# Kernel optimization log

Hardware: AMD Instinct MI355X
Metric: run time of the kernel (lower is better)

Reference implementation:

```python
import jax, jax.numpy as jnp
import numpy as np

# -------- static graph construction (Traffic4cast-style pixel grid) --------
H, W = 495, 436
N = H * W                    # 215820 nodes
D_NODE, D_EDGE, UNITS = 128, 32, 128
UQ = UNITS // 4              # per-quadrant width (combination='concat')
SCALE = 1.0 / 4.0            # 1/(max_neighbors+1)

def _first_occ_unique(v):
    """tf.unique semantics: unique values in first-occurrence order + idx map."""
    u, first, inv = np.unique(v, return_index=True, return_inverse=True)
    order = np.argsort(first)
    rank = np.empty(len(u), dtype=np.int64)
    rank[order] = np.arange(len(u))
    return u[order], rank[inv]

def _build_graph():
    r, c = np.meshgrid(np.arange(H), np.arange(W), indexing='ij')
    node_loc = np.stack([r.ravel(), c.ravel()], -1).astype(np.int64)
    def grid_edges(r0, r1, c0, c1, dr, dc):
        rr, cc = np.meshgrid(np.arange(r0, r1), np.arange(c0, c1), indexing='ij')
        src = (rr * W + cc).ravel()
        dst = ((rr + dr) * W + (cc + dc)).ravel()
        return np.stack([src, dst], -1).astype(np.int64)
    eis = [grid_edges(1, H, 0, W, -1, 0),   # north
           grid_edges(0, H, 0, W - 1, 0, 1),# east
           grid_edges(0, H - 1, 0, W, 1, 0),# south
           grid_edges(0, H, 1, W, 0, -1)]   # west
    return node_loc, eis

NODE_LOC, EIS = _build_graph()

# --- graph_pooling_2x2 bucketing (col_idx=0): pos_id = (r//2)*half_cols + c//2 ---
_half_cols = NODE_LOC[:, 0].max() + 1
_pos_id = (NODE_LOC // 2 * np.array([_half_cols, 1])).sum(-1)
_, NEW_NODE_IDS = _first_occ_unique(_pos_id)
N_POOLED = int(NEW_NODE_IDS.max()) + 1

# --- remove_duplicate_edges precompute per direction (static, int-only) ---
EDGE_SEG, K_UNIQ, KEEP_IDX, NEW_EIDX = [], [], [], []
for _ei in EIS:
    _pe = NEW_NODE_IDS[_ei]
    _lin = _pe[:, 0] * N + _pe[:, 1]
    _u, _seg = _first_occ_unique(_lin)
    _ne = np.stack([_u // N, _u % N], -1)
    _keep = np.where(_ne[:, 0] != _ne[:, 1])[0]
    EDGE_SEG.append(_seg)
    K_UNIQ.append(len(_u))
    KEEP_IDX.append(_keep)
    NEW_EIDX.append(_ne[_keep])


def setup_inputs() -> dict:
    key = jax.random.key(0)
    ks = jax.random.split(key, 9)
    inp = {
        'x': jax.random.normal(ks[0], (N, D_NODE), dtype=jnp.float32),
        'node_loc': jnp.asarray(NODE_LOC),
        'edge_index_n': jnp.asarray(EIS[0]),
        'edge_index_e': jnp.asarray(EIS[1]),
        'edge_index_s': jnp.asarray(EIS[2]),
        'edge_index_w': jnp.asarray(EIS[3]),
        'edges_n': jax.random.uniform(ks[1], (EIS[0].shape[0], D_EDGE), dtype=jnp.float32),
        'edges_e': jax.random.uniform(ks[2], (EIS[1].shape[0], D_EDGE), dtype=jnp.float32),
        'edges_s': jax.random.uniform(ks[3], (EIS[2].shape[0], D_EDGE), dtype=jnp.float32),
        'edges_w': jax.random.uniform(ks[4], (EIS[3].shape[0], D_EDGE), dtype=jnp.float32),
        'W_emb': jax.random.normal(ks[5], (4, D_NODE, UQ), dtype=jnp.float32) * 0.05,
        'W_edge': jax.random.normal(ks[6], (4, D_EDGE + 2 * UQ, UQ), dtype=jnp.float32) * 0.05,
        'W_node': jax.random.normal(ks[7], (D_NODE + UNITS, UNITS), dtype=jnp.float32) * 0.05,
    }
    return inp


def reference(x, node_loc, edge_index_n, edge_index_e, edge_index_s, edge_index_w,
              edges_n, edges_e, edges_s, edges_w, W_emb, W_edge, W_node):
    n = x.shape[0]
    eis = (edge_index_n, edge_index_e, edge_index_s, edge_index_w)
    efs = (edges_n, edges_e, edges_s, edges_w)
    aggs, quad_edges = [], []
    # GeoQuadrantGCN.call_concat (use_global=False, use_bias=False, relu)
    for q in range(4):
        ei = eis[q]
        xq = jax.nn.relu(x @ W_emb[q])                              # [N, UQ]
        edge_in = jnp.concatenate([efs[q], xq[ei[:, 0]], xq[ei[:, 1]]], axis=-1)
        edge = jax.nn.relu(edge_in @ W_edge[q])                     # [E, UQ]
        aggs.append(jax.ops.segment_sum(edge, ei[:, 1], num_segments=n) * SCALE)
        quad_edges.append(edge)
    x2 = jax.nn.relu(jnp.concatenate([x] + aggs, axis=-1) @ W_node) # [N, UNITS]
    # graph_pooling_2x2
    x_pooled = jax.ops.segment_max(x2, jnp.asarray(NEW_NODE_IDS), num_segments=N_POOLED)
    new_pos = jax.ops.segment_min(node_loc // 2, jnp.asarray(NEW_NODE_IDS), num_segments=N_POOLED)
    new_efeats = [
        jax.ops.segment_max(quad_edges[q], jnp.asarray(EDGE_SEG[q]), num_segments=K_UNIQ[q])[KEEP_IDX[q]]
        for q in range(4)
    ]
    new_eidx = [jnp.asarray(NEW_EIDX[q]) for q in range(4)]
    return (x_pooled, new_pos, *new_eidx, *new_efeats)
```

## Files before the change

### kernel.cpp

```cpp
#include <hip/hip_runtime.h>

#define NN 215820
#define NPOOL 54064
#define KN 53846
#define KE 53816

static constexpr size_t OFF_POS = (size_t)NPOOL * 128;
static constexpr size_t OFF_EIN = OFF_POS + (size_t)NPOOL * 2;
static constexpr size_t OFF_EIE = OFF_EIN + (size_t)KN * 2;
static constexpr size_t OFF_EIS = OFF_EIE + (size_t)KE * 2;
static constexpr size_t OFF_EIW = OFF_EIS + (size_t)KN * 2;
static constexpr size_t OFF_EFN = OFF_EIW + (size_t)KE * 2;
static constexpr size_t OFF_EFE = OFF_EFN + (size_t)KN * 32;
static constexpr size_t OFF_EFS = OFF_EFE + (size_t)KE * 32;
static constexpr size_t OFF_EFW = OFF_EFS + (size_t)KN * 32;

typedef __attribute__((ext_vector_type(8))) short  short8v;
typedef __attribute__((ext_vector_type(4))) float  floatx4;

__device__ __align__(16) unsigned short g_wn_h[128 * 256];
__device__ __align__(16) unsigned short g_wn_l[128 * 256];

__device__ __forceinline__ void bf16split(float x, unsigned short& h,
                                          unsigned short& l) {
  const unsigned int u = __float_as_uint(x);
  h = (unsigned short)(u >> 16);
  const float hf = __uint_as_float(u & 0xffff0000u);
  l = (unsigned short)(__float_as_uint(x - hf) >> 16);
}

__device__ __forceinline__ void gemm_chunk(const float* __restrict__ xs,
                                           const float* __restrict__ ws,
                                           const float* const xr[8],
                                           int tx4, float acc[8][8]) {
#pragma unroll 1
  for (int kb = 0; kb < 32; kb += 4) {
    float4 xv[8];
#pragma unroll
    for (int i = 0; i < 8; ++i) xv[i] = *(const float4*)(xr[i] + kb);
    float4 wl[4], wh[4];
#pragma unroll
    for (int kk = 0; kk < 4; ++kk) {
      wl[kk] = *(const float4*)(ws + (kb + kk) * 132 + tx4);
      wh[kk] = *(const float4*)(ws + (kb + kk) * 132 + tx4 + 64);
    }
#pragma unroll
    for (int i = 0; i < 8; ++i) {
      const float* xe = (const float*)&xv[i];
#pragma unroll
      for (int kk = 0; kk < 4; ++kk) {
        acc[i][0] = fmaf(xe[kk], wl[kk].x, acc[i][0]);
        acc[i][1] = fmaf(xe[kk], wl[kk].y, acc[i][1]);
        acc[i][2] = fmaf(xe[kk], wl[kk].z, acc[i][2]);
        acc[i][3] = fmaf(xe[kk], wl[kk].w, acc[i][3]);
        acc[i][4] = fmaf(xe[kk], wh[kk].x, acc[i][4]);
        acc[i][5] = fmaf(xe[kk], wh[kk].y, acc[i][5]);
        acc[i][6] = fmaf(xe[kk], wh[kk].z, acc[i][6]);
        acc[i][7] = fmaf(xe[kk], wh[kk].w, acc[i][7]);
      }
    }
  }
}

__global__ __launch_bounds__(256) void k_xq(const float* __restrict__ x,
                                            const float* __restrict__ W_emb,
                                            float* __restrict__ xq) {
  __shared__ float xs[128 * 36];
  __shared__ float ws[32 * 132];
  const int t  = threadIdx.x;
  const int tx = t & 15, ty = t >> 4;
  const int n0 = blockIdx.x * 128;
  const int srow = t >> 1, soff = (t & 1) * 16;
  int snode = n0 + srow; if (snode >= NN) snode = NN - 1;
  const float* sxa = x + (size_t)snode * 128 + soff;
  float* sxd = xs + srow * 36 + soff;

  int rowidx[8];
#pragma unroll
  for (int i = 0; i < 4; ++i) { rowidx[i] = 4 * ty + i; rowidx[4 + i] = 64 + 4 * ty + i; }
  const float* xr[8];
#pragma unroll
  for (int i = 0; i < 8; ++i) xr[i] = xs + rowidx[i] * 36;
  const int tx4 = tx * 4;

  float acc[8][8];
#pragma unroll
  for (int i = 0; i < 8; ++i)
#pragma unroll
    for (int j = 0; j < 8; ++j) acc[i][j] = 0.f;

  for (int kc = 0; kc < 4; ++kc) {
    __syncthreads();
#pragma unroll
    for (int i = 0; i < 4; ++i)
      *(float4*)(sxd + 4 * i) = *(const float4*)(sxa + kc * 32 + 4 * i);
#pragma unroll
    for (int i = 0; i < 4; ++i) {
      const int f = t * 16 + 4 * i, kk = f >> 7, c = f & 127;
      *(float4*)(ws + kk * 132 + c) =
          *(const float4*)(W_emb + (size_t)(c >> 5) * 4096 +
                           (size_t)(kc * 32 + kk) * 32 + (c & 31));
    }
    __syncthreads();
    gemm_chunk(xs, ws, xr, tx4, acc);
  }
  const int qlo = tx >> 3, ulo = tx4 & 31;
#pragma unroll
  for (int i = 0; i < 8; ++i) {
    const int n = n0 + rowidx[i];
    if (n < NN) {
      float4 v, u;
      v.x = fmaxf(acc[i][0], 0.f); v.y = fmaxf(acc[i][1], 0.f);
      v.z = fmaxf(acc[i][2], 0.f); v.w = fmaxf(acc[i][3], 0.f);
      u.x = fmaxf(acc[i][4], 0.f); u.y = fmaxf(acc[i][5], 0.f);
      u.z = fmaxf(acc[i][6], 0.f); u.w = fmaxf(acc[i][7], 0.f);
      *(float4*)(xq + ((size_t)qlo * NN + n) * 32 + ulo) = v;
      *(float4*)(xq + ((size_t)(qlo + 2) * NN + n) * 32 + ulo) = u;
    }
  }
}

__global__ __launch_bounds__(256, 4) void k_node(const float* __restrict__ x,
                                                 const float* __restrict__ agg,
                                                 float* __restrict__ out) {
  __shared__ short As_h[128 * 32], As_l[128 * 32];
  __shared__ short Bs_h[128 * 32], Bs_l[128 * 32];
  const int t   = threadIdx.x;
  const int pr  = blockIdx.y;
  const int pc0 = blockIdx.x * 32;

  const int srow = t >> 1, q0 = t & 1;
  int ra = (srow < 64) ? 2 * pr : 2 * pr + 1; if (ra > 494) ra = 494;
  int ca = 2 * pc0 + (srow & 63);          if (ca > 435) ca = 435;
  const size_t snode = (size_t)ra * 436 + ca;

  const int w = t >> 6, lane = t & 63;
  const int lr = lane & 15, lg = lane >> 4;

  floatx4 acc[2][8];
#pragma unroll
  for (int mi = 0; mi < 2; ++mi)
#pragma unroll
    for (int ni = 0; ni < 8; ++ni) acc[mi][ni] = (floatx4){0.f, 0.f, 0.f, 0.f};

  for (int ks = 0; ks < 8; ++ks) {
    __syncthreads();
    const float* src = (ks < 4) ? (x + snode * 128 + ks * 32)
                                : (agg + snode * 128 + (ks - 4) * 32);
#pragma unroll
    for (int cc = 0; cc < 2; ++cc) {
      const int q = q0 + 2 * cc;
      const floatx4 v0 = *(const floatx4*)(src + q * 8);
      const floatx4 v1 = *(const floatx4*)(src + q * 8 + 4);
      short8v hv, lv;
#pragma unroll
      for (int j = 0; j < 4; ++j) {
        unsigned short h, l;
        bf16split(v0[j], h, l); hv[j] = (short)h; lv[j] = (short)l;
        bf16split(v1[j], h, l); hv[4 + j] = (short)h; lv[4 + j] = (short)l;
      }
      const int off = srow * 64 + ((q * 16) ^ ((srow & 3) << 4));
      *(short8v*)((char*)As_h + off) = hv;
      *(short8v*)((char*)As_l + off) = lv;
      const size_t wb = (size_t)srow * 256 + ks * 32 + q * 8;
      *(short8v*)((char*)Bs_h + off) = *(const short8v*)(g_wn_h + wb);
      *(short8v*)((char*)Bs_l + off) = *(const short8v*)(g_wn_l + wb);
    }
    __syncthreads();
    short8v ah[2], al[2];
#pragma unroll
    for (int mi = 0; mi < 2; ++mi) {
      const int row = (mi ? 64 : 0) + 16 * w + lr;
      const int off = row * 64 + ((lg * 16) ^ ((row & 3) << 4));
      ah[mi] = *(const short8v*)((const char*)As_h + off);
      al[mi] = *(const short8v*)((const char*)As_l + off);
    }
#pragma unroll
    for (int ni = 0; ni < 8; ++ni) {
      const int col = 16 * ni + lr;
      const int off = col * 64 + ((lg * 16) ^ ((col & 3) << 4));
      const short8v bh = *(const short8v*)((const char*)Bs_h + off);
      const short8v bl = *(const short8v*)((const char*)Bs_l + off);
#pragma unroll
      for (int mi = 0; mi < 2; ++mi) {
        acc[mi][ni] = __builtin_amdgcn_mfma_f32_16x16x32_bf16(ah[mi], bh, acc[mi][ni], 0, 0, 0);
        acc[mi][ni] = __builtin_amdgcn_mfma_f32_16x16x32_bf16(ah[mi], bl, acc[mi][ni], 0, 0, 0);
        acc[mi][ni] = __builtin_amdgcn_mfma_f32_16x16x32_bf16(al[mi], bh, acc[mi][ni], 0, 0, 0);
      }
    }
  }
#pragma unroll
  for (int ni = 0; ni < 8; ++ni) {
#pragma unroll
    for (int k = 0; k < 2; ++k) {
      float v = fmaxf(fmaxf(acc[0][ni][2 * k], acc[0][ni][2 * k + 1]),
                      fmaxf(acc[1][ni][2 * k], acc[1][ni][2 * k + 1]));
      v = fmaxf(v, 0.f);
      const int pc = pc0 + 8 * w + 2 * lg + k;
      if (pc < 218) out[((size_t)pr * 218 + pc) * 128 + 16 * ni + lr] = v;
    }
  }
}

__global__ __launch_bounds__(256) void k_edge(
    const float* __restrict__ ef_n, const float* __restrict__ ef_e,
    const float* __restrict__ ef_s, const float* __restrict__ ef_w,
    const float* __restrict__ xq, const float* __restrict__ W_edge,
    float* __restrict__ agg, float* __restrict__ out) {
  const int q = blockIdx.y;
  const float* ef; float* efb; int P;
  if (q == 0)      { ef = ef_n; P = 107692; efb = out + OFF_EFN; }
  else if (q == 1) { ef = ef_e; P = 107880; efb = out + OFF_EFE; }
  else if (q == 2) { ef = ef_s; P = 107692; efb = out + OFF_EFS; }
  else             { ef = ef_w; P = 107880; efb = out + OFF_EFW; }
  const int j = threadIdx.x & 31, slot = threadIdx.x >> 5;
  const float* Wq = W_edge + q * 3072;
  float wcol[96];
#pragma unroll
  for (int k = 0; k < 96; ++k) wcol[k] = Wq[k * 32 + j];
  const float* xqq = xq + (size_t)q * NN * 32;
  __shared__ float ein[8][192];
  float* row = ein[slot];

  for (int p = blockIdx.x * 8 + slot; p < P; p += gridDim.x * 8) {
    int e1, src1, dst1, e2, src2, dst2, kidx; bool kept, has2;
    if (q == 0) {
      const int rp = p / 218, pc = p - rp * 218;
      const int r = rp + 1, c = 2 * pc;
      e1 = (r - 1) * 436 + c; e2 = e1 + 1;
      src1 = r * 436 + c; dst1 = src1 - 436;
      src2 = src1 + 1; dst2 = dst1 + 1; has2 = true;
      kept = (r & 1) == 0; kidx = ((r >> 1) - 1) * 218 + pc;
    } else if (q == 2) {
      const int r = p / 218, pc = p - r * 218;
      const int c = 2 * pc;
      e1 = r * 436 + c; e2 = e1 + 1;
      src1 = e1; dst1 = src1 + 436;
      src2 = src1 + 1; dst2 = dst1 + 1; has2 = true;
      kept = (r & 1) == 1; kidx = (r >> 1) * 218 + pc;
    } else if (q == 1) {
      const int pr = p / 435, c = p - pr * 435;
      e1 = 2 * pr * 435 + c; e2 = e1 + 435;
      src1 = 2 * pr * 436 + c; dst1 = src1 + 1;
      src2 = src1 + 436; dst2 = dst1 + 436;
      has2 = pr < 247;
      kept = (c & 1) == 1; kidx = pr * 217 + (c >> 1);
    } else {
      const int pr = p / 435, cm = p - pr * 435;
      const int c = cm + 1;
      e1 = 2 * pr * 435 + cm; e2 = e1 + 435;
      src1 = 2 * pr * 436 + c; dst1 = src1 - 1;
      src2 = src1 + 436; dst2 = dst1 + 436;
      has2 = pr < 247;
      kept = (c & 1) == 0; kidx = pr * 217 + (c >> 1) - 1;
    }
    const int e2c = has2 ? e2 : e1;
    const int s2c = has2 ? src2 : src1;
    const int d2c = has2 ? dst2 : dst1;
    row[j]       = ef[(size_t)e1 * 32 + j];
    row[32 + j]  = xqq[(size_t)src1 * 32 + j];
    row[64 + j]  = xqq[(size_t)dst1 * 32 + j];
    row[96 + j]  = ef[(size_t)e2c * 32 + j];
    row[128 + j] = xqq[(size_t)s2c * 32 + j];
    row[160 + j] = xqq[(size_t)d2c * 32 + j];
    float a1 = 0.f, a2 = 0.f;
#pragma unroll
    for (int kq = 0; kq < 24; ++kq) {
      const float4 b1 = *(const float4*)&row[4 * kq];
      const float4 b2 = *(const float4*)&row[96 + 4 * kq];
      a1 = fmaf(b1.x, wcol[4 * kq + 0], a1); a1 = fmaf(b1.y, wcol[4 * kq + 1], a1);
      a1 = fmaf(b1.z, wcol[4 * kq + 2], a1); a1 = fmaf(b1.w, wcol[4 * kq + 3], a1);
      a2 = fmaf(b2.x, wcol[4 * kq + 0], a2); a2 = fmaf(b2.y, wcol[4 * kq + 1], a2);
      a2 = fmaf(b2.z, wcol[4 * kq + 2], a2); a2 = fmaf(b2.w, wcol[4 * kq + 3], a2);
    }
    const float f1 = fmaxf(a1, 0.f), f2 = fmaxf(a2, 0.f);
    agg[(size_t)dst1 * 128 + q * 32 + j] = f1 * 0.25f;
    if (has2) agg[(size_t)dst2 * 128 + q * 32 + j] = f2 * 0.25f;
    if (kept) efb[(size_t)kidx * 32 + j] = has2 ? fmaxf(f1, f2) : f1;
  }
}

__global__ __launch_bounds__(256) void k_misc(float* __restrict__ out,
                                              float* __restrict__ agg,
                                              const float* __restrict__ W_node) {
  int u = blockIdx.x * 256 + threadIdx.x;
  if (u < 436 * 32) {
    agg[((size_t)494 * 436 + (u >> 5)) * 128 + (u & 31)] = 0.f; return;
  }
  u -= 436 * 32;
  if (u < 495 * 32) {
    agg[(size_t)(u >> 5) * 436 * 128 + 32 + (u & 31)] = 0.f; return;
  }
  u -= 495 * 32;
  if (u < 436 * 32) {
    agg[(size_t)(u >> 5) * 128 + 64 + (u & 31)] = 0.f; return;
  }
  u -= 436 * 32;
  if (u < 495 * 32) {
    agg[((size_t)(u >> 5) * 436 + 435) * 128 + 96 + (u & 31)] = 0.f; return;
  }
  u -= 495 * 32;
  if (u < NPOOL * 2) {
    const int p  = u >> 1;
    const int pr = p / 218, pc = p - pr * 218;
    out[OFF_POS + u] = (float)((u & 1) ? pc : pr); return;
  }
  u -= NPOOL * 2;
  if (u < KN * 2) {
    const int e  = u >> 1;
    const int kr = e / 218 + 1, pc = e - (kr - 1) * 218;
    const int s  = kr * 218 + pc;
    out[OFF_EIN + u] = (float)((u & 1) ? (s - 218) : s); return;
  }
  u -= KN * 2;
  if (u < KE * 2) {
    const int e  = u >> 1;
    const int pr = e / 217, jj = e - pr * 217;
    const int s  = pr * 218 + jj;
    out[OFF_EIE + u] = (float)((u & 1) ? (s + 1) : s); return;
  }
  u -= KE * 2;
  if (u < KN * 2) {
    const int e  = u >> 1;
    const int k  = e / 218, pc = e - k * 218;
    const int s  = k * 218 + pc;
    out[OFF_EIS + u] = (float)((u & 1) ? (s + 218) : s); return;
  }
  u -= KN * 2;
  if (u < KE * 2) {
    const int e  = u >> 1;
    const int pr = e / 217, jj = e - pr * 217;
    const int s  = pr * 218 + jj + 1;
    out[OFF_EIW + u] = (float)((u & 1) ? (s - 1) : s); return;
  }
  u -= KE * 2;
  if (u < 256 * 128) {
    const int k = u >> 7, c = u & 127;
    unsigned short h, l;
    bf16split(W_node[u], h, l);
    g_wn_h[(size_t)c * 256 + k] = h;
    g_wn_l[(size_t)c * 256 + k] = l;
  }
}

extern "C" void kernel_launch(void* const* d_in, const int* in_sizes, int n_in,
                              void* d_out, int out_size, void* d_ws, size_t ws_size,
                              hipStream_t stream) {
  const float* x      = (const float*)d_in[0];
  const float* ef_n   = (const float*)d_in[6];
  const float* ef_e   = (const float*)d_in[7];
  const float* ef_s   = (const float*)d_in[8];
  const float* ef_w   = (const float*)d_in[9];
  const float* W_emb  = (const float*)d_in[10];
  const float* W_edge = (const float*)d_in[11];
  const float* W_node = (const float*)d_in[12];
  float* out = (float*)d_out;

  float* xq  = (float*)d_ws;
  float* agg = xq + (size_t)NN * 128;

  const int misc_total = (436 + 495 + 436 + 495) * 32 + NPOOL * 2 +
                         2 * (KN * 2 + KE * 2) + 256 * 128;
  k_misc<<<dim3((misc_total + 255) / 256), 256, 0, stream>>>(out, agg, W_node);
  k_xq  <<<dim3((NN + 127) / 128), 256, 0, stream>>>(x, W_emb, xq);
  k_edge<<<dim3(512, 4), 256, 0, stream>>>(ef_n, ef_e, ef_s, ef_w,
                                           xq, W_edge, agg, out);
  k_node<<<dim3(7, 248), 256, 0, stream>>>(x, agg, out);
}
```

Before: 509.7 us.

## Compute node embedding GEMM with split-bf16 MFMA instead of FP32 FMAs

The x @ W_emb kernel is rewritten to use bf16 MFMA instructions with a hi/lo split (three MFMAs per tile) in place of the scalar FP32 FMA tiling. W_emb is pre-split into transposed bf16 hi/lo arrays inside the misc kernel, and x is split on the fly into swizzled shared memory. This moves the embedding GEMM onto the matrix cores while keeping near-FP32 accuracy. In exchange the output stores become scalar rather than float4, and the extra split work adds ALU cost.

```diff
diff --git a/kernel.cpp b/kernel.cpp
--- a/kernel.cpp
+++ b/kernel.cpp
@@ -20,6 +20,8 @@
 
 __device__ __align__(16) unsigned short g_wn_h[128 * 256];
 __device__ __align__(16) unsigned short g_wn_l[128 * 256];
+__device__ __align__(16) unsigned short g_we_h[128 * 128];
+__device__ __align__(16) unsigned short g_we_l[128 * 128];
 
 __device__ __forceinline__ void bf16split(float x, unsigned short& h,
                                           unsigned short& l) {
@@ -29,93 +31,81 @@
   l = (unsigned short)(__float_as_uint(x - hf) >> 16);
 }
 
-__device__ __forceinline__ void gemm_chunk(const float* __restrict__ xs,
-                                           const float* __restrict__ ws,
-                                           const float* const xr[8],
-                                           int tx4, float acc[8][8]) {
-#pragma unroll 1
-  for (int kb = 0; kb < 32; kb += 4) {
-    float4 xv[8];
-#pragma unroll
-    for (int i = 0; i < 8; ++i) xv[i] = *(const float4*)(xr[i] + kb);
-    float4 wl[4], wh[4];
-#pragma unroll
-    for (int kk = 0; kk < 4; ++kk) {
-      wl[kk] = *(const float4*)(ws + (kb + kk) * 132 + tx4);
-      wh[kk] = *(const float4*)(ws + (kb + kk) * 132 + tx4 + 64);
-    }
-#pragma unroll
-    for (int i = 0; i < 8; ++i) {
-      const float* xe = (const float*)&xv[i];
-#pragma unroll
-      for (int kk = 0; kk < 4; ++kk) {
-        acc[i][0] = fmaf(xe[kk], wl[kk].x, acc[i][0]);
-        acc[i][1] = fmaf(xe[kk], wl[kk].y, acc[i][1]);
-        acc[i][2] = fmaf(xe[kk], wl[kk].z, acc[i][2]);
-        acc[i][3] = fmaf(xe[kk], wl[kk].w, acc[i][3]);
-        acc[i][4] = fmaf(xe[kk], wh[kk].x, acc[i][4]);
-        acc[i][5] = fmaf(xe[kk], wh[kk].y, acc[i][5]);
-        acc[i][6] = fmaf(xe[kk], wh[kk].z, acc[i][6]);
-        acc[i][7] = fmaf(xe[kk], wh[kk].w, acc[i][7]);
-      }
-    }
-  }
-}
-
-__global__ __launch_bounds__(256) void k_xq(const float* __restrict__ x,
-                                            const float* __restrict__ W_emb,
-                                            float* __restrict__ xq) {
-  __shared__ float xs[128 * 36];
-  __shared__ float ws[32 * 132];
+__global__ __launch_bounds__(256, 4) void k_xq(const float* __restrict__ x,
+                                               float* __restrict__ xq) {
+  __shared__ __align__(16) short As_h[128 * 32], As_l[128 * 32];
+  __shared__ __align__(16) short Bs_h[128 * 32], Bs_l[128 * 32];
   const int t  = threadIdx.x;
-  const int tx = t & 15, ty = t >> 4;
   const int n0 = blockIdx.x * 128;
-  const int srow = t >> 1, soff = (t & 1) * 16;
-  int snode = n0 + srow; if (snode >= NN) snode = NN - 1;
-  const float* sxa = x + (size_t)snode * 128 + soff;
-  float* sxd = xs + srow * 36 + soff;
-
-  int rowidx[8];
-#pragma unroll
-  for (int i = 0; i < 4; ++i) { rowidx[i] = 4 * ty + i; rowidx[4 + i] = 64 + 4 * ty + i; }
-  const float* xr[8];
-#pragma unroll
-  for (int i = 0; i < 8; ++i) xr[i] = xs + rowidx[i] * 36;
-  const int tx4 = tx * 4;
-
-  float acc[8][8];
-#pragma unroll
-  for (int i = 0; i < 8; ++i)
-#pragma unroll
-    for (int j = 0; j < 8; ++j) acc[i][j] = 0.f;
-
-  for (int kc = 0; kc < 4; ++kc) {
+  const int srow = t >> 1, q0 = t & 1;
+  int sn = n0 + srow; if (sn >= NN) sn = NN - 1;
+  const float* srcx = x + (size_t)sn * 128;
+  const int w = t >> 6, lane = t & 63;
+  const int lr = lane & 15, lg = lane >> 4;
+
+  floatx4 acc[2][8];
+#pragma unroll
+  for (int mi = 0; mi < 2; ++mi)
+#pragma unroll
+    for (int ni = 0; ni < 8; ++ni) acc[mi][ni] = (floatx4){0.f, 0.f, 0.f, 0.f};
+
+  for (int ks = 0; ks < 4; ++ks) {
     __syncthreads();
 #pragma unroll
-    for (int i = 0; i < 4; ++i)
-      *(float4*)(sxd + 4 * i) = *(const float4*)(sxa + kc * 32 + 4 * i);
-#pragma unroll
-    for (int i = 0; i < 4; ++i) {
-      const int f = t * 16 + 4 * i, kk = f >> 7, c = f & 127;
-      *(float4*)(ws + kk * 132 + c) =
-          *(const float4*)(W_emb + (size_t)(c >> 5) * 4096 +
-                           (size_t)(kc * 32 + kk) * 32 + (c & 31));
+    for (int cc = 0; cc < 2; ++cc) {
+      const int q = q0 + 2 * cc;
+      const floatx4 v0 = *(const floatx4*)(srcx + ks * 32 + q * 8);
+      const floatx4 v1 = *(const floatx4*)(srcx + ks * 32 + q * 8 + 4);
+      short8v hv, lv;
+#pragma unroll
+      for (int j = 0; j < 4; ++j) {
+        unsigned short h, l;
+        bf16split(v0[j], h, l); hv[j] = (short)h; lv[j] = (short)l;
+        bf16split(v1[j], h, l); hv[4 + j] = (short)h; lv[4 + j] = (short)l;
+      }
+      const int off = srow * 64 + ((q * 16) ^ ((srow & 3) << 4));
+      *(short8v*)((char*)As_h + off) = hv;
+      *(short8v*)((char*)As_l + off) = lv;
+      const size_t wb = (size_t)srow * 128 + ks * 32 + q * 8;
+      *(short8v*)((char*)Bs_h + off) = *(const short8v*)(g_we_h + wb);
+      *(short8v*)((char*)Bs_l + off) = *(const short8v*)(g_we_l + wb);
     }
     __syncthreads();
-    gemm_chunk(xs, ws, xr, tx4, acc);
-  }
-  const int qlo = tx >> 3, ulo = tx4 & 31;
-#pragma unroll
-  for (int i = 0; i < 8; ++i) {
-    const int n = n0 + rowidx[i];
-    if (n < NN) {
-      float4 v, u;
-      v.x = fmaxf(acc[i][0], 0.f); v.y = fmaxf(acc[i][1], 0.f);
-      v.z = fmaxf(acc[i][2], 0.f); v.w = fmaxf(acc[i][3], 0.f);
-      u.x = fmaxf(acc[i][4], 0.f); u.y = fmaxf(acc[i][5], 0.f);
-      u.z = fmaxf(acc[i][6], 0.f); u.w = fmaxf(acc[i][7], 0.f);
-      *(float4*)(xq + ((size_t)qlo * NN + n) * 32 + ulo) = v;
-      *(float4*)(xq + ((size_t)(qlo + 2) * NN + n) * 32 + ulo) = u;
+    short8v ah[2], al[2];
+#pragma unroll
+    for (int mi = 0; mi < 2; ++mi) {
+      const int row = (mi ? 64 : 0) + 16 * w + lr;
+      const int off = row * 64 + ((lg * 16) ^ ((row & 3) << 4));
+      ah[mi] = *(const short8v*)((const char*)As_h + off);
+      al[mi] = *(const short8v*)((const char*)As_l + off);
+    }
+#pragma unroll
+    for (int ni = 0; ni < 8; ++ni) {
+      const int col = 16 * ni + lr;
+      const int off = col * 64 + ((lg * 16) ^ ((col & 3) << 4));
+      const short8v bh = *(const short8v*)((const char*)Bs_h + off);
+      const short8v bl = *(const short8v*)((const char*)Bs_l + off);
+#pragma unroll
+      for (int mi = 0; mi < 2; ++mi) {
+        acc[mi][ni] = __builtin_amdgcn_mfma_f32_16x16x32_bf16(ah[mi], bh, acc[mi][ni], 0, 0, 0);
+        acc[mi][ni] = __builtin_amdgcn_mfma_f32_16x16x32_bf16(ah[mi], bl, acc[mi][ni], 0, 0, 0);
+        acc[mi][ni] = __builtin_amdgcn_mfma_f32_16x16x32_bf16(al[mi], bh, acc[mi][ni], 0, 0, 0);
+      }
+    }
+  }
+#pragma unroll
+  for (int ni = 0; ni < 8; ++ni) {
+    const int col = 16 * ni + lr;
+    const int qq = col >> 5, u = col & 31;
+#pragma unroll
+    for (int mi = 0; mi < 2; ++mi) {
+      const int nb = n0 + (mi ? 64 : 0) + 16 * w + 4 * lg;
+#pragma unroll
+      for (int r = 0; r < 4; ++r) {
+        const int n = nb + r;
+        if (n < NN)
+          xq[((size_t)qq * NN + n) * 32 + u] = fmaxf(acc[mi][ni][r], 0.f);
+      }
     }
   }
 }
@@ -282,7 +272,8 @@
 
 __global__ __launch_bounds__(256) void k_misc(float* __restrict__ out,
                                               float* __restrict__ agg,
-                                              const float* __restrict__ W_node) {
+                                              const float* __restrict__ W_node,
+                                              const float* __restrict__ W_emb) {
   int u = blockIdx.x * 256 + threadIdx.x;
   if (u < 436 * 32) {
     agg[((size_t)494 * 436 + (u >> 5)) * 128 + (u & 31)] = 0.f; return;
@@ -340,6 +331,15 @@
     bf16split(W_node[u], h, l);
     g_wn_h[(size_t)c * 256 + k] = h;
     g_wn_l[(size_t)c * 256 + k] = l;
+    return;
+  }
+  u -= 256 * 128;
+  if (u < 4 * 128 * 32) {
+    const int q = u >> 12, k = (u >> 5) & 127, uu = u & 31;
+    unsigned short h, l;
+    bf16split(W_emb[u], h, l);
+    g_we_h[(size_t)(q * 32 + uu) * 128 + k] = h;
+    g_we_l[(size_t)(q * 32 + uu) * 128 + k] = l;
   }
 }
 
@@ -360,9 +360,10 @@
   float* agg = xq + (size_t)NN * 128;
 
   const int misc_total = (436 + 495 + 436 + 495) * 32 + NPOOL * 2 +
-                         2 * (KN * 2 + KE * 2) + 256 * 128;
-  k_misc<<<dim3((misc_total + 255) / 256), 256, 0, stream>>>(out, agg, W_node);
-  k_xq  <<<dim3((NN + 127) / 128), 256, 0, stream>>>(x, W_emb, xq);
+                         2 * (KN * 2 + KE * 2) + 256 * 128 + 4 * 128 * 32;
+  k_misc<<<dim3((misc_total + 255) / 256), 256, 0, stream>>>(out, agg,
+                                                             W_node, W_emb);
+  k_xq  <<<dim3((NN + 127) / 128), 256, 0, stream>>>(x, xq);
   k_edge<<<dim3(512, 4), 256, 0, stream>>>(ef_n, ef_e, ef_s, ef_w,
                                            xq, W_edge, agg, out);
   k_node<<<dim3(7, 248), 256, 0, stream>>>(x, agg, out);
```

Measured after the change: 467.0 us. 1.09x faster.
